# Kernel tuning notes

Measured on AMD Instinct MI355X. Metric: run time of the kernel, lower is better.

Reference implementation:

```python
import jax, jax.numpy as jnp
import numpy as np

DECAY = 0.99


def setup_inputs() -> dict:
    key = jax.random.key(0)
    k1, k2 = jax.random.split(key)
    N, D = 8192, 3
    target = jax.random.normal(k1, (1, N, D), dtype=jnp.float32)
    output = jax.random.normal(k2, (1, N, D), dtype=jnp.float32)
    return {"target": target, "output": output, "cur": 190, "substeps": 19}


def reference(target, output, cur, substeps):
    # target, output: (1, N, 3) point clouds.
    a = target[0]  # (N, 3)
    b = output[0]  # (M, 3)
    # Squared pairwise distances via ||a||^2 + ||b||^2 - 2 a.b^T  -> (N, M)
    a2 = jnp.sum(a * a, axis=-1)  # (N,)
    b2 = jnp.sum(b * b, axis=-1)  # (M,)
    d2 = a2[:, None] + b2[None, :] - 2.0 * jnp.einsum('nd,md->nm', a, b)
    d2 = jnp.maximum(d2, 0.0)  # clamp numerical negatives
    dist1 = jnp.min(d2, axis=1)  # nearest output point for each target point, squared
    dist2 = jnp.min(d2, axis=0)  # nearest target point for each output point, squared
    loss = (jnp.mean(jnp.sqrt(dist1)) + jnp.mean(jnp.sqrt(dist2))) * 0.5
    scale = 10.0 / (DECAY ** (cur // substeps))
    return loss * scale
```

## Files before the change

kernel.cpp:

```cpp
#include <hip/hip_runtime.h>
#include <math.h>

#define N      8192
#define BLK    256
#define RPT    4
#define G      (RPT / 2)
#define BPW    (64 * RPT)
#define NB     (N / BPW)
#define NA     (N / 64)
#define GRID   ((NB * NA) / 4)
#define RBLK   1024
#define RGRID  8

typedef float v2f __attribute__((ext_vector_type(2)));

__device__ __forceinline__ float rot1(float x) {
    return __int_as_float(__builtin_amdgcn_mov_dpp(
        __float_as_int(x), 0x13C, 0xF, 0xF, false));
}

__global__ __launch_bounds__(BLK) void chamfer_prep_kernel(
        const float* __restrict__ tgt, const float* __restrict__ outp,
        float4* __restrict__ P, unsigned* __restrict__ dmin) {
    int i = blockIdx.x * BLK + (int)threadIdx.x;
    const float* src = (i < N) ? tgt : outp;
    int k = (i < N) ? i : (i - N);
    float x = src[3 * k + 0];
    float y = src[3 * k + 1];
    float z = src[3 * k + 2];
    P[i] = make_float4(x, y, z, fmaf(x, x, fmaf(y, y, z * z)));
    dmin[i] = 0x7F800000u;
}

__global__ __launch_bounds__(BLK) void chamfer_dist_kernel(
        const float4* __restrict__ P, unsigned* __restrict__ dmin) {
    __shared__ unsigned cm[BPW];

    int tid  = (int)threadIdx.x;
    int lane = tid & 63;
    int W    = (int)blockIdx.x * 4 + (tid >> 6);
    int bt   = W >> 7;
    int at   = W & (NA - 1);

    cm[tid] = 0x7F800000u;

    v2f bx2[G], by2[G], bz2[G], b22[G], ca2[G];
    #pragma unroll
    for (int g = 0; g < G; ++g) {
        float4 u = P[N + bt * BPW + (2 * g)     * 64 + lane];
        float4 v = P[N + bt * BPW + (2 * g + 1) * 64 + lane];
        bx2[g] = (v2f){u.x, v.x};
        by2[g] = (v2f){u.y, v.y};
        bz2[g] = (v2f){u.z, v.z};
        b22[g] = (v2f){u.w, v.w};
        ca2[g] = (v2f){__builtin_inff(), __builtin_inff()};
    }

    float4 a = P[at * 64 + lane];
    float px = -2.0f * a.x;
    float py = -2.0f * a.y;
    float pz = -2.0f * a.z;
    float pw = a.w;
    float pr = __builtin_inff();

    __syncthreads();

    for (int s = 0; s < 64; ++s) {
        v2f px2 = {px, px}, py2 = {py, py}, pz2 = {pz, pz}, pw2 = {pw, pw};
        #pragma unroll
        for (int g = 0; g < G; ++g) {
            v2f t = __builtin_elementwise_fma(pz2, bz2[g], b22[g] + pw2);
            t     = __builtin_elementwise_fma(py2, by2[g], t);
            t     = __builtin_elementwise_fma(px2, bx2[g], t);
            pr     = fminf(fminf(pr, t.x), t.y);
            ca2[g] = __builtin_elementwise_min(ca2[g], t);
        }
        px = rot1(px);
        py = rot1(py);
        pz = rot1(pz);
        pw = rot1(pw);
        pr = rot1(pr);
    }

    atomicMin(&dmin[at * 64 + lane], __float_as_uint(fmaxf(pr, 0.0f)));

    #pragma unroll
    for (int g = 0; g < G; ++g) {
        atomicMin(&cm[(2 * g)     * 64 + lane],
                  __float_as_uint(fmaxf(ca2[g].x, 0.0f)));
        atomicMin(&cm[(2 * g + 1) * 64 + lane],
                  __float_as_uint(fmaxf(ca2[g].y, 0.0f)));
    }
    __syncthreads();
    atomicMin(&dmin[N + bt * BPW + tid], cm[tid]);
}

__global__ __launch_bounds__(RBLK) void chamfer_reduce_kernel(
        const unsigned* __restrict__ dmin, float* __restrict__ bsum) {
    __shared__ float sh1[RBLK / 64], sh2[RBLK / 64];
    int t = (int)threadIdx.x;
    int chunk = N / 4 / RGRID;
    int base = (int)blockIdx.x * chunk;
    float s1 = 0.0f, s2 = 0.0f;
    const uint4* da = (const uint4*)dmin;
    const uint4* db = (const uint4*)(dmin + N);
    for (int i = t; i < chunk; i += RBLK) {
        uint4 v1 = da[base + i], v2 = db[base + i];
        s1 += sqrtf(__uint_as_float(v1.x)) + sqrtf(__uint_as_float(v1.y))
            + sqrtf(__uint_as_float(v1.z)) + sqrtf(__uint_as_float(v1.w));
        s2 += sqrtf(__uint_as_float(v2.x)) + sqrtf(__uint_as_float(v2.y))
            + sqrtf(__uint_as_float(v2.z)) + sqrtf(__uint_as_float(v2.w));
    }
    #pragma unroll
    for (int off = 32; off > 0; off >>= 1) {
        s1 += __shfl_down(s1, off, 64);
        s2 += __shfl_down(s2, off, 64);
    }
    int wid = t >> 6, lane = t & 63;
    if (lane == 0) { sh1[wid] = s1; sh2[wid] = s2; }
    __syncthreads();
    if (t == 0) {
        float t1 = 0.0f, t2 = 0.0f;
        #pragma unroll
        for (int w = 0; w < RBLK / 64; ++w) { t1 += sh1[w]; t2 += sh2[w]; }
        bsum[blockIdx.x]         = t1;
        bsum[RGRID + blockIdx.x] = t2;
    }
}

__global__ void chamfer_final_kernel(const float* __restrict__ bsum,
        const int* __restrict__ curp, const int* __restrict__ subp,
        float* __restrict__ out) {
    if (threadIdx.x != 0) return;
    float s1 = 0.0f, s2 = 0.0f;
    #pragma unroll
    for (int b = 0; b < RGRID; ++b) { s1 += bsum[b]; s2 += bsum[RGRID + b]; }
    int e = curp[0] / subp[0];
    double scale = 10.0 / pow(0.99, (double)e);
    out[0] = (float)((((double)s1 + (double)s2) / (double)N) * 0.5 * scale);
}

extern "C" void kernel_launch(void* const* d_in, const int* in_sizes, int n_in,
                              void* d_out, int out_size, void* d_ws, size_t ws_size,
                              hipStream_t stream) {
    const float* target = (const float*)d_in[0];
    const float* output = (const float*)d_in[1];
    const int*   curp   = (const int*)d_in[2];
    const int*   subp   = (const int*)d_in[3];
    float* out = (float*)d_out;

    float4*   P    = (float4*)d_ws;
    unsigned* dmin = (unsigned*)(P + 2 * N);
    float*    bsum = (float*)(dmin + 2 * N);

    chamfer_prep_kernel<<<2 * N / BLK, BLK, 0, stream>>>(target, output, P, dmin);
    chamfer_dist_kernel<<<GRID, BLK, 0, stream>>>(P, dmin);
    chamfer_reduce_kernel<<<RGRID, RBLK, 0, stream>>>(dmin, bsum);
    chamfer_final_kernel<<<1, 64, 0, stream>>>(bsum, curp, subp, out);
}
```

Before: 23.48 us.

## Fuse point preprocessing into distance kernel and double per-lane output tile

Drops the separate prep kernel. The distance kernel now reads the raw xyz arrays and computes squared norms in registers, and the min buffer is initialised with an async memset. Each wave also covers twice as many output points (RPT 4→8), which halves the grid and the atomic traffic for target minima. The trade-off is more strided, uncoalesced loads of the 3-float points and higher register pressure per thread.

```diff
diff --git a/kernel.cpp b/kernel.cpp
--- a/kernel.cpp
+++ b/kernel.cpp
@@ -3,7 +3,7 @@
 
 #define N      8192
 #define BLK    256
-#define RPT    4
+#define RPT    8
 #define G      (RPT / 2)
 #define BPW    (64 * RPT)
 #define NB     (N / BPW)
@@ -19,21 +19,9 @@
         __float_as_int(x), 0x13C, 0xF, 0xF, false));
 }
 
-__global__ __launch_bounds__(BLK) void chamfer_prep_kernel(
+__global__ __launch_bounds__(BLK) void chamfer_dist_kernel(
         const float* __restrict__ tgt, const float* __restrict__ outp,
-        float4* __restrict__ P, unsigned* __restrict__ dmin) {
-    int i = blockIdx.x * BLK + (int)threadIdx.x;
-    const float* src = (i < N) ? tgt : outp;
-    int k = (i < N) ? i : (i - N);
-    float x = src[3 * k + 0];
-    float y = src[3 * k + 1];
-    float z = src[3 * k + 2];
-    P[i] = make_float4(x, y, z, fmaf(x, x, fmaf(y, y, z * z)));
-    dmin[i] = 0x7F800000u;
-}
-
-__global__ __launch_bounds__(BLK) void chamfer_dist_kernel(
-        const float4* __restrict__ P, unsigned* __restrict__ dmin) {
+        unsigned* __restrict__ dmin) {
     __shared__ unsigned cm[BPW];
 
     int tid  = (int)threadIdx.x;
@@ -42,25 +30,30 @@
     int bt   = W >> 7;
     int at   = W & (NA - 1);
 
-    cm[tid] = 0x7F800000u;
+    cm[tid]       = 0x7F800000u;
+    cm[tid + 256] = 0x7F800000u;
 
     v2f bx2[G], by2[G], bz2[G], b22[G], ca2[G];
     #pragma unroll
     for (int g = 0; g < G; ++g) {
-        float4 u = P[N + bt * BPW + (2 * g)     * 64 + lane];
-        float4 v = P[N + bt * BPW + (2 * g + 1) * 64 + lane];
-        bx2[g] = (v2f){u.x, v.x};
-        by2[g] = (v2f){u.y, v.y};
-        bz2[g] = (v2f){u.z, v.z};
-        b22[g] = (v2f){u.w, v.w};
+        int j0 = bt * BPW + (2 * g)     * 64 + lane;
+        int j1 = bt * BPW + (2 * g + 1) * 64 + lane;
+        float ux = outp[3 * j0 + 0], uy = outp[3 * j0 + 1], uz = outp[3 * j0 + 2];
+        float vx = outp[3 * j1 + 0], vy = outp[3 * j1 + 1], vz = outp[3 * j1 + 2];
+        bx2[g] = (v2f){ux, vx};
+        by2[g] = (v2f){uy, vy};
+        bz2[g] = (v2f){uz, vz};
+        b22[g] = (v2f){fmaf(ux, ux, fmaf(uy, uy, uz * uz)),
+                       fmaf(vx, vx, fmaf(vy, vy, vz * vz))};
         ca2[g] = (v2f){__builtin_inff(), __builtin_inff()};
     }
 
-    float4 a = P[at * 64 + lane];
-    float px = -2.0f * a.x;
-    float py = -2.0f * a.y;
-    float pz = -2.0f * a.z;
-    float pw = a.w;
+    int ia = at * 64 + lane;
+    float axr = tgt[3 * ia + 0], ayr = tgt[3 * ia + 1], azr = tgt[3 * ia + 2];
+    float px = -2.0f * axr;
+    float py = -2.0f * ayr;
+    float pz = -2.0f * azr;
+    float pw = fmaf(axr, axr, fmaf(ayr, ayr, azr * azr));
     float pr = __builtin_inff();
 
     __syncthreads();
@@ -92,7 +85,8 @@
                   __float_as_uint(fmaxf(ca2[g].y, 0.0f)));
     }
     __syncthreads();
-    atomicMin(&dmin[N + bt * BPW + tid], cm[tid]);
+    atomicMin(&dmin[N + bt * BPW + tid],       cm[tid]);
+    atomicMin(&dmin[N + bt * BPW + tid + 256], cm[tid + 256]);
 }
 
 __global__ __launch_bounds__(RBLK) void chamfer_reduce_kernel(
@@ -149,12 +143,11 @@
     const int*   subp   = (const int*)d_in[3];
     float* out = (float*)d_out;
 
-    float4*   P    = (float4*)d_ws;
-    unsigned* dmin = (unsigned*)(P + 2 * N);
+    unsigned* dmin = (unsigned*)d_ws;
     float*    bsum = (float*)(dmin + 2 * N);
 
-    chamfer_prep_kernel<<<2 * N / BLK, BLK, 0, stream>>>(target, output, P, dmin);
-    chamfer_dist_kernel<<<GRID, BLK, 0, stream>>>(P, dmin);
+    hipMemsetD32Async((hipDeviceptr_t)dmin, 0x7F800000, 2 * N, stream);
+    chamfer_dist_kernel<<<GRID, BLK, 0, stream>>>(target, output, dmin);
     chamfer_reduce_kernel<<<RGRID, RBLK, 0, stream>>>(dmin, bsum);
     chamfer_final_kernel<<<1, 64, 0, stream>>>(bsum, curp, subp, out);
 }
```

After: 22.90 us. -2.5%, faster.
